# Optimization experiments

Hardware: AMD Instinct MI355X
Metric: run time of the kernel (lower is better)

Reference implementation:

```python
import jax, jax.numpy as jnp
import numpy as np

N_USER = 100000
N_ITEM = 50000
N_NODES = N_USER + N_ITEM
NNZ = 3000000
N_LAYERS = 3
BATCH = 4096
EMB = 64


def setup_inputs() -> dict:
    key = jax.random.key(0)
    ks = jax.random.split(key, 8)
    return {
        "user_emb": jax.random.normal(ks[0], (N_USER, EMB), dtype=jnp.float32) * 0.1,
        "item_emb": jax.random.normal(ks[1], (N_ITEM, EMB), dtype=jnp.float32) * 0.1,
        "adj_vals": jax.random.uniform(ks[2], (NNZ,), dtype=jnp.float32) * 0.05,
        "adj_rows": jax.random.randint(ks[3], (NNZ,), 0, N_NODES, dtype=jnp.int32),
        "adj_cols": jax.random.randint(ks[4], (NNZ,), 0, N_NODES, dtype=jnp.int32),
        "users": jax.random.randint(ks[5], (BATCH,), 0, N_USER, dtype=jnp.int32),
        "pos_items": jax.random.randint(ks[6], (BATCH,), 0, N_ITEM, dtype=jnp.int32),
        "neg_items": jax.random.randint(ks[7], (BATCH,), 0, N_ITEM, dtype=jnp.int32),
    }


def _spmm(vals, rows, cols, x):
    # sparse [N,N] @ dense [N,D] via gather + segment-sum
    return jax.ops.segment_sum(vals[:, None] * x[cols], rows, num_segments=N_NODES)


def reference(user_emb, item_emb, adj_vals, adj_rows, adj_cols, users, pos_items, neg_items):
    ego = jnp.concatenate([user_emb, item_emb], axis=0)  # [N, D]
    acc = ego
    cur = ego
    for _ in range(N_LAYERS):
        cur = _spmm(adj_vals, adj_rows, adj_cols, cur)
        acc = acc + cur
    all_emb = acc / (N_LAYERS + 1)  # mean over stacked layer outputs
    u_g = all_emb[:N_USER]
    i_g = all_emb[N_USER:]
    return (u_g[users], i_g[pos_items], i_g[neg_items])
```

## Files before the change

kernel.cpp:

```cpp
#include <hip/hip_runtime.h>
#include <hip/hip_fp16.h>

#define EMB_C 64
#define N_USER_C 100000
#define BROWS 256
#define BSHIFT 8
#define COLBITS 18
#define NBMAX 640


__global__ __launch_bounds__(256) void fill_h_kernel(
        const float4* __restrict__ ue, const float4* __restrict__ ie,
        ushort4* __restrict__ x0, long long u4, long long t4) {
    long long i = (long long)blockIdx.x * blockDim.x + threadIdx.x;
    if (i >= t4) return;
    float4 v = (i < u4) ? ue[i] : ie[i - u4];
    ushort4 h;
    h.x = __half_as_ushort(__float2half(v.x));
    h.y = __half_as_ushort(__float2half(v.y));
    h.z = __half_as_ushort(__float2half(v.z));
    h.w = __half_as_ushort(__float2half(v.w));
    x0[i] = h;
}

__global__ __launch_bounds__(256) void chunkhist_kernel(
        const int* __restrict__ rows, int* __restrict__ ghist, int nnz, int nb,
        int csz) {
    __shared__ int hist[NBMAX];
    for (int b = threadIdx.x; b < nb; b += 256) hist[b] = 0;
    __syncthreads();
    const long long c0 = (long long)blockIdx.x * csz;
    for (int i = threadIdx.x; i < csz; i += 256) {
        long long e = c0 + i;
        if (e < nnz) atomicAdd(&hist[rows[e] >> BSHIFT], 1);
    }
    __syncthreads();
    for (int b = threadIdx.x; b < nb; b += 256)
        ghist[blockIdx.x * NBMAX + b] = hist[b];
}

__global__ __launch_bounds__(256) void colscan_kernel(
        int* __restrict__ ghist, int* __restrict__ btot, int NC, int nb) {
    __shared__ int sh[256];
    const int b = blockIdx.x;
    int run = 0;
    for (int c0 = 0; c0 < NC; c0 += 256) {
        int c = c0 + threadIdx.x;
        int v = (c < NC) ? ghist[c * NBMAX + b] : 0;
        sh[threadIdx.x] = v;
        __syncthreads();
        for (int off = 1; off < 256; off <<= 1) {
            int t = (threadIdx.x >= off) ? sh[threadIdx.x - off] : 0;
            __syncthreads();
            sh[threadIdx.x] += t;
            __syncthreads();
        }
        if (c < NC) ghist[c * NBMAX + b] = run + sh[threadIdx.x] - v;
        run += sh[255];
        __syncthreads();
    }
    if (threadIdx.x == 0) btot[b] = run;
}

__global__ __launch_bounds__(1024) void bucketscan_kernel(
        const int* __restrict__ btot, int* __restrict__ bbase,
        int* __restrict__ rp, int nb, int nnz, int n_nodes) {
    __shared__ int sh[1024];
    int v = (threadIdx.x < nb) ? btot[threadIdx.x] : 0;
    sh[threadIdx.x] = v;
    __syncthreads();
    for (int off = 1; off < 1024; off <<= 1) {
        int t = (threadIdx.x >= off) ? sh[threadIdx.x - off] : 0;
        __syncthreads();
        sh[threadIdx.x] += t;
        __syncthreads();
    }
    if (threadIdx.x < nb) bbase[threadIdx.x] = sh[threadIdx.x] - v;
    if (threadIdx.x == 0) { bbase[nb] = nnz; rp[n_nodes] = nnz; }
}

__global__ __launch_bounds__(256) void binscatter2_kernel(
        const int* __restrict__ rows, const int* __restrict__ cols,
        const float* __restrict__ vals, const int* __restrict__ ghist,
        const int* __restrict__ bbase, int2* __restrict__ bin, int nnz, int nb,
        int csz) {
    __shared__ int cur[NBMAX];
    const int chunk = blockIdx.x;
    const long long c0 = (long long)chunk * csz;
    for (int b = threadIdx.x; b < nb; b += 256)
        cur[b] = bbase[b] + ghist[chunk * NBMAX + b];
    __syncthreads();
    for (int i = threadIdx.x; i < csz; i += 256) {
        long long e = c0 + i;
        if (e >= nnz) break;
        int r = rows[e];
        int b = r >> BSHIFT;
        int k = atomicAdd(&cur[b], 1);
        bin[k] = make_int2(((r & (BROWS - 1)) << COLBITS) | cols[e],
                           __float_as_int(vals[e]));
    }
}

__global__ __launch_bounds__(512) void finscatter_kernel(
        const int2* __restrict__ bin, const int* __restrict__ bbase,
        int* __restrict__ rp, int2* __restrict__ sce, int n_nodes) {
    __shared__ int cnt[BROWS];
    __shared__ int sh[BROWS];
    __shared__ int cur[BROWS];
    const int row0 = blockIdx.x << BSHIFT;
    const int tid = threadIdx.x;
    if (tid < BROWS) cnt[tid] = 0;
    __syncthreads();
    const int bb = bbase[blockIdx.x];
    const int be = bbase[blockIdx.x + 1];
    for (int p = bb + tid; p < be; p += 512)
        atomicAdd(&cnt[bin[p].x >> COLBITS], 1);
    __syncthreads();
    int v = 0;
    if (tid < BROWS) { v = cnt[tid]; sh[tid] = v; }
    __syncthreads();
    for (int off = 1; off < BROWS; off <<= 1) {
        int t = (tid < BROWS && tid >= off) ? sh[tid - off] : 0;
        __syncthreads();
        if (tid < BROWS) sh[tid] += t;
        __syncthreads();
    }
    if (tid < BROWS) {
        int excl = sh[tid] - v;
        cur[tid] = excl;
        if (row0 + tid < n_nodes) rp[row0 + tid] = bb + excl;
    }
    __syncthreads();
    for (int p = bb + tid; p < be; p += 512) {
        int2 e = bin[p];
        int rl = e.x >> COLBITS;
        int k = atomicAdd(&cur[rl], 1);
        sce[bb + k] = make_int2(e.x & ((1 << COLBITS) - 1), e.y);
    }
}

__global__ __launch_bounds__(256) void spmm_h_kernel(
        const int* __restrict__ rp, const int2* __restrict__ sce,
        const __half* __restrict__ xin, __half* __restrict__ xnxt,
        int n_nodes) {
    int wid = (int)(((long long)blockIdx.x * blockDim.x + threadIdx.x) >> 6);
    int lane = threadIdx.x & 63;
    if (wid >= n_nodes) return;
    int beg = __builtin_amdgcn_readfirstlane(rp[wid]);
    int end = __builtin_amdgcn_readfirstlane(rp[wid + 1]);
    const unsigned long long* __restrict__ sceq = (const unsigned long long*)sce;
    float s0 = 0.f, s1 = 0.f, s2 = 0.f, s3 = 0.f;
    int p = beg;
    for (; p + 8 <= end; p += 8) {
        unsigned long long u0 = __builtin_nontemporal_load(sceq + p + 0);
        unsigned long long u1 = __builtin_nontemporal_load(sceq + p + 1);
        unsigned long long u2 = __builtin_nontemporal_load(sceq + p + 2);
        unsigned long long u3 = __builtin_nontemporal_load(sceq + p + 3);
        unsigned long long u4 = __builtin_nontemporal_load(sceq + p + 4);
        unsigned long long u5 = __builtin_nontemporal_load(sceq + p + 5);
        unsigned long long u6 = __builtin_nontemporal_load(sceq + p + 6);
        unsigned long long u7 = __builtin_nontemporal_load(sceq + p + 7);
        float g0 = __half2float(xin[((int)(unsigned)u0) * EMB_C + lane]);
        float g1 = __half2float(xin[((int)(unsigned)u1) * EMB_C + lane]);
        float g2 = __half2float(xin[((int)(unsigned)u2) * EMB_C + lane]);
        float g3 = __half2float(xin[((int)(unsigned)u3) * EMB_C + lane]);
        float g4 = __half2float(xin[((int)(unsigned)u4) * EMB_C + lane]);
        float g5 = __half2float(xin[((int)(unsigned)u5) * EMB_C + lane]);
        float g6 = __half2float(xin[((int)(unsigned)u6) * EMB_C + lane]);
        float g7 = __half2float(xin[((int)(unsigned)u7) * EMB_C + lane]);
        s0 = fmaf(__int_as_float((int)(u0 >> 32)), g0, s0);
        s1 = fmaf(__int_as_float((int)(u1 >> 32)), g1, s1);
        s2 = fmaf(__int_as_float((int)(u2 >> 32)), g2, s2);
        s3 = fmaf(__int_as_float((int)(u3 >> 32)), g3, s3);
        s0 = fmaf(__int_as_float((int)(u4 >> 32)), g4, s0);
        s1 = fmaf(__int_as_float((int)(u5 >> 32)), g5, s1);
        s2 = fmaf(__int_as_float((int)(u6 >> 32)), g6, s2);
        s3 = fmaf(__int_as_float((int)(u7 >> 32)), g7, s3);
    }
    for (; p + 4 <= end; p += 4) {
        unsigned long long u0 = __builtin_nontemporal_load(sceq + p + 0);
        unsigned long long u1 = __builtin_nontemporal_load(sceq + p + 1);
        unsigned long long u2 = __builtin_nontemporal_load(sceq + p + 2);
        unsigned long long u3 = __builtin_nontemporal_load(sceq + p + 3);
        float g0 = __half2float(xin[((int)(unsigned)u0) * EMB_C + lane]);
        float g1 = __half2float(xin[((int)(unsigned)u1) * EMB_C + lane]);
        float g2 = __half2float(xin[((int)(unsigned)u2) * EMB_C + lane]);
        float g3 = __half2float(xin[((int)(unsigned)u3) * EMB_C + lane]);
        s0 = fmaf(__int_as_float((int)(u0 >> 32)), g0, s0);
        s1 = fmaf(__int_as_float((int)(u1 >> 32)), g1, s1);
        s2 = fmaf(__int_as_float((int)(u2 >> 32)), g2, s2);
        s3 = fmaf(__int_as_float((int)(u3 >> 32)), g3, s3);
    }
    for (; p < end; ++p) {
        unsigned long long u = __builtin_nontemporal_load(sceq + p);
        s0 = fmaf(__int_as_float((int)(u >> 32)),
                  __half2float(xin[((int)(unsigned)u) * EMB_C + lane]), s0);
    }
    float s = (s0 + s1) + (s2 + s3);
    unsigned short hs = __half_as_ushort(__float2half(s));
    __builtin_nontemporal_store(hs, (unsigned short*)(xnxt + wid * EMB_C + lane));
}

__global__ __launch_bounds__(256) void gather_h_kernel(
        const __half* __restrict__ p0, const __half* __restrict__ p1,
        const __half* __restrict__ p2, const __half* __restrict__ p3,
        const int* __restrict__ users, const int* __restrict__ pos,
        const int* __restrict__ neg, float* __restrict__ out,
        int batch, float scale) {
    long long gid = (long long)blockIdx.x * blockDim.x + threadIdx.x;
    long long per = (long long)batch * EMB_C;
    if (gid >= 3 * per) return;
    int which = (int)(gid / per);
    long long rem = gid - (long long)which * per;
    int b = (int)(rem >> 6);
    int d = (int)(rem & 63);
    long long row;
    if (which == 0)      row = users[b];
    else if (which == 1) row = (long long)N_USER_C + pos[b];
    else                 row = (long long)N_USER_C + neg[b];
    long long idx = row * EMB_C + d;
    out[gid] = scale * (__half2float(p0[idx]) + __half2float(p1[idx]) +
                        __half2float(p2[idx]) + __half2float(p3[idx]));
}


__global__ __launch_bounds__(256) void fill_kernel(
        const float4* __restrict__ ue, const float4* __restrict__ ie,
        float4* __restrict__ x0, float4* __restrict__ a,
        float4* __restrict__ b, long long u4, long long t4) {
    long long i = (long long)blockIdx.x * blockDim.x + threadIdx.x;
    if (i >= t4) return;
    float4 v = (i < u4) ? ue[i] : ie[i - u4];
    x0[i] = v;
    a[i] = v;
    b[i] = make_float4(0.f, 0.f, 0.f, 0.f);
}

__global__ __launch_bounds__(256) void spmm_kernel(
        const float* __restrict__ vals, const int* __restrict__ rows,
        const int* __restrict__ cols, const float* __restrict__ xin,
        float* __restrict__ xout, int nnz) {
    long long gid = (long long)blockIdx.x * blockDim.x + threadIdx.x;
    int e = (int)(gid >> 6);
    int d = (int)(gid & 63);
    if (e >= nnz) return;
    unsafeAtomicAdd(&xout[(long long)rows[e] * EMB_C + d],
                    vals[e] * xin[(long long)cols[e] * EMB_C + d]);
}

__global__ __launch_bounds__(256) void acczero_kernel(
        float4* __restrict__ acc, const float4* __restrict__ src,
        float4* __restrict__ tozero, long long n4) {
    long long i = (long long)blockIdx.x * blockDim.x + threadIdx.x;
    if (i >= n4) return;
    float4 a = acc[i], s = src[i];
    a.x += s.x; a.y += s.y; a.z += s.z; a.w += s.w;
    acc[i] = a;
    if (tozero) tozero[i] = make_float4(0.f, 0.f, 0.f, 0.f);
}

__global__ __launch_bounds__(256) void gather_f_kernel(
        const float* __restrict__ acc,
        const int* __restrict__ users, const int* __restrict__ pos,
        const int* __restrict__ neg, float* __restrict__ out,
        int batch, float scale) {
    long long gid = (long long)blockIdx.x * blockDim.x + threadIdx.x;
    long long per = (long long)batch * EMB_C;
    if (gid >= 3 * per) return;
    int which = (int)(gid / per);
    long long rem = gid - (long long)which * per;
    int b = (int)(rem >> 6);
    int d = (int)(rem & 63);
    long long row;
    if (which == 0)      row = users[b];
    else if (which == 1) row = (long long)N_USER_C + pos[b];
    else                 row = (long long)N_USER_C + neg[b];
    out[gid] = scale * acc[row * EMB_C + d];
}


extern "C" void kernel_launch(void* const* d_in, const int* in_sizes, int n_in,
                              void* d_out, int out_size, void* d_ws, size_t ws_size,
                              hipStream_t stream) {
    const float* ue    = (const float*)d_in[0];
    const float* ie    = (const float*)d_in[1];
    const float* vals  = (const float*)d_in[2];
    const int*   rows  = (const int*)d_in[3];
    const int*   cols  = (const int*)d_in[4];
    const int*   users = (const int*)d_in[5];
    const int*   pos   = (const int*)d_in[6];
    const int*   neg   = (const int*)d_in[7];
    float* out = (float*)d_out;

    const int nnz   = in_sizes[2];
    const int batch = in_sizes[5];
    const long long uelems = (long long)in_sizes[0];
    const long long total  = uelems + (long long)in_sizes[1];
    const int n_nodes = (int)(total / EMB_C);
    const long long u4 = uelems / 4, t4 = total / 4;

    const int T = 256;
    const int fill_blocks = (int)((t4 + T - 1) / T);
    const int gath_blocks = (int)((3LL * batch * EMB_C + T - 1) / T);
    const int spmm_blocks = (int)(((long long)n_nodes * EMB_C + T - 1) / T);
    const int nb = (n_nodes + BROWS - 1) / BROWS;

    const long long RN = ((n_nodes + 1 + 15) / 16) * 16;
    const size_t xbytes = (size_t)total * 2;
    const size_t fixed = 4 * xbytes + (size_t)(RN + 2048) * 4 + (size_t)nnz * 16;
    const bool fits_nb = (nb <= NBMAX) && (n_nodes <= (1 << COLBITS));

    int csz = 2048;
    int NC = (nnz + csz - 1) / csz;
    if (!fits_nb || ws_size < fixed + (size_t)NC * NBMAX * 4) {
        csz = 8192;
        NC = (nnz + csz - 1) / csz;
    }
    const size_t needH = fixed + (size_t)NC * NBMAX * 4;

    char* wb = (char*)d_ws;

    if (fits_nb && ws_size >= needH) {
        __half* x0 = (__half*)wb;
        __half* x1 = (__half*)(wb + xbytes);
        __half* x2 = (__half*)(wb + 2 * xbytes);
        __half* x3 = (__half*)(wb + 3 * xbytes);
        int*   rp    = (int*)(wb + 4 * xbytes);
        int*   btot  = rp + RN;
        int*   bbase = btot + 1024;
        int*   ghist = bbase + 1024;
        int2*  sce   = (int2*)(ghist + (size_t)NC * NBMAX);
        int2*  bin   = sce + nnz;

        fill_h_kernel<<<fill_blocks, T, 0, stream>>>(
            (const float4*)ue, (const float4*)ie, (ushort4*)x0, u4, t4);

        chunkhist_kernel<<<NC, T, 0, stream>>>(rows, ghist, nnz, nb, csz);
        colscan_kernel<<<nb, T, 0, stream>>>(ghist, btot, NC, nb);
        bucketscan_kernel<<<1, 1024, 0, stream>>>(btot, bbase, rp, nb, nnz, n_nodes);
        binscatter2_kernel<<<NC, T, 0, stream>>>(rows, cols, vals, ghist, bbase,
                                                 bin, nnz, nb, csz);
        finscatter_kernel<<<nb, 512, 0, stream>>>(bin, bbase, rp, sce, n_nodes);

        spmm_h_kernel<<<spmm_blocks, T, 0, stream>>>(rp, sce, x0, x1, n_nodes);
        spmm_h_kernel<<<spmm_blocks, T, 0, stream>>>(rp, sce, x1, x2, n_nodes);
        spmm_h_kernel<<<spmm_blocks, T, 0, stream>>>(rp, sce, x2, x3, n_nodes);

        gather_h_kernel<<<gath_blocks, T, 0, stream>>>(
            x0, x1, x2, x3, users, pos, neg, out, batch, 0.25f);
    } else {
        float* cur = (float*)wb;
        float* nxt = cur + total;
        float* acc = nxt + total;
        fill_kernel<<<fill_blocks, T, 0, stream>>>(
            (const float4*)ue, (const float4*)ie,
            (float4*)cur, (float4*)acc, (float4*)nxt, u4, t4);
        const int espmm_blocks = (int)(((long long)nnz * EMB_C + T - 1) / T);
        for (int l = 0; l < 3; ++l) {
            spmm_kernel<<<espmm_blocks, T, 0, stream>>>(vals, rows, cols, cur, nxt, nnz);
            float4* tz = (l < 2) ? (float4*)cur : nullptr;
            acczero_kernel<<<fill_blocks, T, 0, stream>>>(
                (float4*)acc, (const float4*)nxt, tz, t4);
            float* t = cur; cur = nxt; nxt = t;
        }
        gather_f_kernel<<<gath_blocks, T, 0, stream>>>(
            acc, users, pos, neg, out, batch, 0.0625f);
    }
}
```

Baseline: 441.9 us.

## Split wavefront into two half-waves each gathering packed half2 rows per edge

The SpMM kernel now has each 64-lane wavefront handle two edges at a time. Each half-wave of 32 lanes loads one neighbor row as 32 packed half2 words instead of 64 scalar halves. The two partial sums are combined with a cross-half shuffle, and the result is written as half2 by the lower 32 lanes. This halves the number of gather instructions per edge and uses wider 4-byte loads, at the cost of a shuffle reduction, an odd-edge tail that masks out the upper half, and idle lanes during the store.

```diff
diff --git a/kernel.cpp b/kernel.cpp
--- a/kernel.cpp
+++ b/kernel.cpp
@@ -139,7 +139,7 @@
     }
 }
 
-__global__ __launch_bounds__(256) void spmm_h_kernel(
+__global__ __launch_bounds__(256) void spmm_h2_kernel(
         const int* __restrict__ rp, const int2* __restrict__ sce,
         const __half* __restrict__ xin, __half* __restrict__ xnxt,
         int n_nodes) {
@@ -148,57 +148,53 @@
     if (wid >= n_nodes) return;
     int beg = __builtin_amdgcn_readfirstlane(rp[wid]);
     int end = __builtin_amdgcn_readfirstlane(rp[wid + 1]);
-    const unsigned long long* __restrict__ sceq = (const unsigned long long*)sce;
-    float s0 = 0.f, s1 = 0.f, s2 = 0.f, s3 = 0.f;
+    const unsigned long long* __restrict__ sq = (const unsigned long long*)sce;
+    const unsigned int* __restrict__ x2 = (const unsigned int*)xin;
+    const int hsel = lane >> 5;
+    const int dp = lane & 31;
+    float l0 = 0.f, h0 = 0.f, l1 = 0.f, h1 = 0.f;
     int p = beg;
     for (; p + 8 <= end; p += 8) {
-        unsigned long long u0 = __builtin_nontemporal_load(sceq + p + 0);
-        unsigned long long u1 = __builtin_nontemporal_load(sceq + p + 1);
-        unsigned long long u2 = __builtin_nontemporal_load(sceq + p + 2);
-        unsigned long long u3 = __builtin_nontemporal_load(sceq + p + 3);
-        unsigned long long u4 = __builtin_nontemporal_load(sceq + p + 4);
-        unsigned long long u5 = __builtin_nontemporal_load(sceq + p + 5);
-        unsigned long long u6 = __builtin_nontemporal_load(sceq + p + 6);
-        unsigned long long u7 = __builtin_nontemporal_load(sceq + p + 7);
-        float g0 = __half2float(xin[((int)(unsigned)u0) * EMB_C + lane]);
-        float g1 = __half2float(xin[((int)(unsigned)u1) * EMB_C + lane]);
-        float g2 = __half2float(xin[((int)(unsigned)u2) * EMB_C + lane]);
-        float g3 = __half2float(xin[((int)(unsigned)u3) * EMB_C + lane]);
-        float g4 = __half2float(xin[((int)(unsigned)u4) * EMB_C + lane]);
-        float g5 = __half2float(xin[((int)(unsigned)u5) * EMB_C + lane]);
-        float g6 = __half2float(xin[((int)(unsigned)u6) * EMB_C + lane]);
-        float g7 = __half2float(xin[((int)(unsigned)u7) * EMB_C + lane]);
-        s0 = fmaf(__int_as_float((int)(u0 >> 32)), g0, s0);
-        s1 = fmaf(__int_as_float((int)(u1 >> 32)), g1, s1);
-        s2 = fmaf(__int_as_float((int)(u2 >> 32)), g2, s2);
-        s3 = fmaf(__int_as_float((int)(u3 >> 32)), g3, s3);
-        s0 = fmaf(__int_as_float((int)(u4 >> 32)), g4, s0);
-        s1 = fmaf(__int_as_float((int)(u5 >> 32)), g5, s1);
-        s2 = fmaf(__int_as_float((int)(u6 >> 32)), g6, s2);
-        s3 = fmaf(__int_as_float((int)(u7 >> 32)), g7, s3);
-    }
-    for (; p + 4 <= end; p += 4) {
-        unsigned long long u0 = __builtin_nontemporal_load(sceq + p + 0);
-        unsigned long long u1 = __builtin_nontemporal_load(sceq + p + 1);
-        unsigned long long u2 = __builtin_nontemporal_load(sceq + p + 2);
-        unsigned long long u3 = __builtin_nontemporal_load(sceq + p + 3);
-        float g0 = __half2float(xin[((int)(unsigned)u0) * EMB_C + lane]);
-        float g1 = __half2float(xin[((int)(unsigned)u1) * EMB_C + lane]);
-        float g2 = __half2float(xin[((int)(unsigned)u2) * EMB_C + lane]);
-        float g3 = __half2float(xin[((int)(unsigned)u3) * EMB_C + lane]);
-        s0 = fmaf(__int_as_float((int)(u0 >> 32)), g0, s0);
-        s1 = fmaf(__int_as_float((int)(u1 >> 32)), g1, s1);
-        s2 = fmaf(__int_as_float((int)(u2 >> 32)), g2, s2);
-        s3 = fmaf(__int_as_float((int)(u3 >> 32)), g3, s3);
-    }
-    for (; p < end; ++p) {
-        unsigned long long u = __builtin_nontemporal_load(sceq + p);
-        s0 = fmaf(__int_as_float((int)(u >> 32)),
-                  __half2float(xin[((int)(unsigned)u) * EMB_C + lane]), s0);
-    }
-    float s = (s0 + s1) + (s2 + s3);
-    unsigned short hs = __half_as_ushort(__float2half(s));
-    __builtin_nontemporal_store(hs, (unsigned short*)(xnxt + wid * EMB_C + lane));
+        unsigned long long u0 = __builtin_nontemporal_load(sq + p + 0 + hsel);
+        unsigned long long u1 = __builtin_nontemporal_load(sq + p + 2 + hsel);
+        unsigned long long u2 = __builtin_nontemporal_load(sq + p + 4 + hsel);
+        unsigned long long u3 = __builtin_nontemporal_load(sq + p + 6 + hsel);
+        unsigned int g0 = x2[((int)(unsigned)u0) * 32 + dp];
+        unsigned int g1 = x2[((int)(unsigned)u1) * 32 + dp];
+        unsigned int g2 = x2[((int)(unsigned)u2) * 32 + dp];
+        unsigned int g3 = x2[((int)(unsigned)u3) * 32 + dp];
+        float v0 = __int_as_float((int)(u0 >> 32));
+        float v1 = __int_as_float((int)(u1 >> 32));
+        float v2 = __int_as_float((int)(u2 >> 32));
+        float v3 = __int_as_float((int)(u3 >> 32));
+        float2 f;
+        f = __half22float2(*(__half2*)&g0); l0 = fmaf(v0, f.x, l0); h0 = fmaf(v0, f.y, h0);
+        f = __half22float2(*(__half2*)&g1); l1 = fmaf(v1, f.x, l1); h1 = fmaf(v1, f.y, h1);
+        f = __half22float2(*(__half2*)&g2); l0 = fmaf(v2, f.x, l0); h0 = fmaf(v2, f.y, h0);
+        f = __half22float2(*(__half2*)&g3); l1 = fmaf(v3, f.x, l1); h1 = fmaf(v3, f.y, h1);
+    }
+    for (; p + 2 <= end; p += 2) {
+        unsigned long long u = __builtin_nontemporal_load(sq + p + hsel);
+        unsigned int g = x2[((int)(unsigned)u) * 32 + dp];
+        float v = __int_as_float((int)(u >> 32));
+        float2 f = __half22float2(*(__half2*)&g);
+        l0 = fmaf(v, f.x, l0); h0 = fmaf(v, f.y, h0);
+    }
+    if (p < end) {
+        unsigned long long u = __builtin_nontemporal_load(sq + p);
+        unsigned int g = x2[((int)(unsigned)u) * 32 + dp];
+        float v = hsel ? 0.f : __int_as_float((int)(u >> 32));
+        float2 f = __half22float2(*(__half2*)&g);
+        l0 = fmaf(v, f.x, l0); h0 = fmaf(v, f.y, h0);
+    }
+    float slo = l0 + l1, shi = h0 + h1;
+    slo += __shfl_xor(slo, 32);
+    shi += __shfl_xor(shi, 32);
+    if (lane < 32) {
+        __half2 hh = __floats2half2_rn(slo, shi);
+        __builtin_nontemporal_store(*(unsigned int*)&hh,
+                                    (unsigned int*)xnxt + wid * 32 + dp);
+    }
 }
 
 __global__ __launch_bounds__(256) void gather_h_kernel(
@@ -342,9 +338,9 @@
                                                  bin, nnz, nb, csz);
         finscatter_kernel<<<nb, 512, 0, stream>>>(bin, bbase, rp, sce, n_nodes);
 
-        spmm_h_kernel<<<spmm_blocks, T, 0, stream>>>(rp, sce, x0, x1, n_nodes);
-        spmm_h_kernel<<<spmm_blocks, T, 0, stream>>>(rp, sce, x1, x2, n_nodes);
-        spmm_h_kernel<<<spmm_blocks, T, 0, stream>>>(rp, sce, x2, x3, n_nodes);
+        spmm_h2_kernel<<<spmm_blocks, T, 0, stream>>>(rp, sce, x0, x1, n_nodes);
+        spmm_h2_kernel<<<spmm_blocks, T, 0, stream>>>(rp, sce, x1, x2, n_nodes);
+        spmm_h2_kernel<<<spmm_blocks, T, 0, stream>>>(rp, sce, x2, x3, n_nodes);
 
         gather_h_kernel<<<gath_blocks, T, 0, stream>>>(
             x0, x1, x2, x3, users, pos, neg, out, batch, 0.25f);
```

Result: slower. 560.5 us (+26.8%).
